# Optimization experiments

Measured on AMD Instinct MI355X. Metric: run time of the kernel, lower is better.

## Reference

```python
import jax, jax.numpy as jnp
import numpy as np

B, L, D = 2, 1024, 1024
H, KV, CH = 16, 4, 8          # attn heads, kv heads, context-manager heads
HD = D // H                   # 64
E, K, FF = 8, 2, 4 * D        # experts, top-k, ffn hidden
DC = 4                        # conv kernel size
EPS = 1e-6


def setup_inputs() -> dict:
    key = jax.random.key(0)
    ks = jax.random.split(key, 32)
    s = 0.02
    n = lambda k, shp: jax.random.normal(k, shp, jnp.float32) * s
    return {
        'x': jax.random.normal(ks[0], (B, L, D), jnp.float32),
        'mask': jnp.ones((B, L), jnp.int32),
        'w_rms1': jnp.ones((D,), jnp.float32),
        'w_rms2': jnp.ones((D,), jnp.float32),
        'w_rms3': jnp.ones((D,), jnp.float32),
        'w_rms4': jnp.ones((D,), jnp.float32),
        'Wq': n(ks[1], (D, D)), 'Wk': n(ks[2], (D, KV * HD)),
        'Wv': n(ks[3], (D, KV * HD)), 'Wo': n(ks[4], (D, D)),
        'Cq': n(ks[5], (D, D)), 'Ck': n(ks[6], (D, D)),
        'Cv': n(ks[7], (D, D)), 'Co': n(ks[8], (D, D)),
        'Wi': n(ks[9], (D, 2 * D)), 'bi': jnp.zeros((2 * D,), jnp.float32),
        'conv_w': n(ks[10], (D, 1, DC)), 'conv_b': jnp.zeros((D,), jnp.float32),
        'Wod': n(ks[11], (D, D)), 'bod': jnp.zeros((D,), jnp.float32),
        'w_gate': n(ks[12], (E, D)),
        'W1': n(ks[13], (E, D, FF)), 'b1': jnp.zeros((E, FF), jnp.float32),
        'W2': n(ks[14], (E, FF, D)), 'b2': jnp.zeros((E, D), jnp.float32),
    }


def _rmsnorm(x, w):
    rms = jnp.sqrt(jnp.mean(x * x, axis=-1, keepdims=True) + EPS)
    return w * (x / rms)


def _mha(x, mask, Wq, Wk, Wv, Wo, nh, nkv):
    b, l, d = x.shape
    hd = d // nh
    q = (x @ Wq).reshape(b, l, nh, hd)
    k = (x @ Wk).reshape(b, l, nkv, hd)
    v = (x @ Wv).reshape(b, l, nkv, hd)
    if nh != nkv:
        rep = nh // nkv
        k = jnp.repeat(k, rep, axis=2)
        v = jnp.repeat(v, rep, axis=2)
    scores = jnp.einsum('bqhd,bkhd->bhqk', q, k) * (hd ** -0.5)
    scores = jnp.where(mask[:, None, None, :] == 0, -jnp.inf, scores)
    attn = jax.nn.softmax(scores, axis=-1)
    out = jnp.einsum('bhqk,bkhd->bqhd', attn, v).reshape(b, l, d)
    return out @ Wo


def _deltanet(x, Wi, bi, conv_w, conv_b, Wod, bod):
    gv = x @ Wi + bi
    gate, value = jnp.split(gv, 2, axis=-1)
    # depthwise causal conv1d (kernel DC, left pad DC-1, truncated to L)
    v_ncl = jnp.transpose(value, (0, 2, 1))  # [B, D, L]
    conv = jax.lax.conv_general_dilated(
        v_ncl, conv_w, window_strides=(1,), padding=[(DC - 1, 0)],
        feature_group_count=D, dimension_numbers=('NCH', 'OIH', 'NCH'))
    conv = conv + conv_b[None, :, None]
    conv = jnp.transpose(conv, (0, 2, 1))  # [B, L, D]
    gated = conv * jax.nn.silu(gate)
    return gated @ Wod + bod


def _moe(x, w_gate, W1, b1, W2, b2):
    b, l, d = x.shape
    flat = x.reshape(-1, d)                                  # [T, D]
    gate = jax.nn.softmax(flat @ w_gate.T, axis=-1)          # [T, E]
    topk_scores, topk_idx = jax.lax.top_k(gate, K)           # [T, K]
    onehot = jax.nn.one_hot(topk_idx, E, dtype=flat.dtype)   # [T, K, E]
    combine = jnp.sum(topk_scores[..., None] * onehot, axis=1)  # [T, E]
    h = jnp.einsum('td,edh->teh', flat, W1) + b1
    h = jax.nn.gelu(h, approximate=False)
    y = jnp.einsum('teh,ehd->ted', h, W2) + b2
    out = jnp.einsum('ted,te->td', y, combine)
    return out.reshape(b, l, d)


def reference(x, mask, w_rms1, w_rms2, w_rms3, w_rms4,
              Wq, Wk, Wv, Wo, Cq, Ck, Cv, Co,
              Wi, bi, conv_w, conv_b, Wod, bod,
              w_gate, W1, b1, W2, b2):
    # eval mode: dropout = identity. multi_token_pred output is discarded by the block.
    res1 = x
    h = _rmsnorm(x, w_rms1)
    h = res1 + _mha(h, mask, Wq, Wk, Wv, Wo, H, KV)
    res2 = h
    # ContextManager stand-in: 8-head softmax self-attention (source unavailable)
    cm = _mha(h, mask, Cq, Ck, Cv, Co, CH, CH)
    h = res2 + cm
    res3 = h
    g = _rmsnorm(h, w_rms2)
    h = res3 + _deltanet(g, Wi, bi, conv_w, conv_b, Wod, bod)
    res4 = h
    g = _rmsnorm(h, w_rms3)
    h = res4 + _moe(g, w_gate, W1, b1, W2, b2)
    h = _rmsnorm(h, w_rms4)
    return h
```

## Files before the change

kernel.cpp:

```cpp
#include <hip/hip_runtime.h>
#include <hip/hip_bf16.h>
#include <math.h>

#define T_TOK 2048
#define B_SZ 2
#define L_SEQ 1024
#define D_MOD 1024
#define N_H 16
#define N_KV 4
#define N_CH 8
#define N_E 8
#define FF_DIM 4096
#define DC_K 4
#define EPS_F 1e-6f

typedef unsigned short u16;
typedef unsigned int u32;
typedef short s16x8 __attribute__((ext_vector_type(8)));
typedef u16 u16x8 __attribute__((ext_vector_type(8)));
typedef float f32x4 __attribute__((ext_vector_type(4)));
struct alignas(8) U16x4 { u16 a, b, c, d; };

__device__ __forceinline__ float gelu_exact(float x) {
    return 0.5f * x * (1.0f + erff(x * 0.70710678118654752f));
}
__device__ __forceinline__ u16 f2bf(float f) {
    u32 x = __float_as_uint(f);
    return (u16)((x + 0x7fffu + ((x >> 16) & 1u)) >> 16);
}
__device__ __forceinline__ float b2f(u16 u) {
    return __uint_as_float(((u32)u) << 16);
}
__device__ __forceinline__ void gload_lds16(const u16* g, u16* l) {
    __builtin_amdgcn_global_load_lds(
        (const __attribute__((address_space(1))) u32*)g,
        (__attribute__((address_space(3))) u32*)l, 16, 0, 0);
}
__device__ __forceinline__ int swz(int row, int ch, int cpr) {
    return (cpr == 4) ? (ch ^ ((row >> 1) & 3)) : (ch ^ (row & 7));
}

struct TDesc {
    const float* src;
    u16* dst;
    int R, C, dstStride, dstRowOff, tileBase, nPerMat;
};
struct TPack { TDesc d[10]; };

__global__ __launch_bounds__(256) void transpose_all(TPack p) {
    __shared__ float ts[64][65];
    int t = blockIdx.x;
    int i = 0;
#pragma unroll
    for (int j = 1; j < 10; ++j)
        if (t >= p.d[j].tileBase) i = j;
    TDesc d = p.d[i];
    int local = t - d.tileBase;
    int e = local / d.nPerMat;
    local -= e * d.nPerMat;
    int ntx = d.C >> 6;
    int bx = local % ntx, by = local / ntx;
    const float* src = d.src + (size_t)e * d.R * d.C + (size_t)(by * 64) * d.C + bx * 64;
    u16* dst = d.dst + (size_t)e * d.C * d.dstStride +
               (size_t)(d.dstRowOff + bx * 64) * d.dstStride + by * 64;
    int tid = threadIdx.x;
#pragma unroll
    for (int k = 0; k < 4; ++k) {
        int fidx = k * 256 + tid;
        int r = fidx >> 4, c4 = (fidx & 15) << 2;
        float4 v = *(const float4*)(src + (size_t)r * d.C + c4);
        ts[r][c4] = v.x; ts[r][c4 + 1] = v.y; ts[r][c4 + 2] = v.z; ts[r][c4 + 3] = v.w;
    }
    __syncthreads();
#pragma unroll
    for (int k = 0; k < 2; ++k) {
        int idx = k * 256 + tid;
        int c = idx >> 3, r8 = (idx & 7) << 3;
        u16x8 o;
#pragma unroll
        for (int j = 0; j < 8; ++j) o[j] = f2bf(ts[r8 + j][c]);
        *(u16x8*)(dst + (size_t)c * d.dstStride + r8) = o;
    }
}

__global__ __launch_bounds__(256) void rmsnorm_kernel(const float* __restrict__ x,
                                                      const float* __restrict__ w,
                                                      float* __restrict__ fo,
                                                      u16* __restrict__ bo) {
    int row = blockIdx.x;
    int tid = threadIdx.x;
    const float* xr = x + (size_t)row * D_MOD;
    float4 v = ((const float4*)xr)[tid];
    float ss = v.x * v.x + v.y * v.y + v.z * v.z + v.w * v.w;
    __shared__ float red[256];
    red[tid] = ss;
    __syncthreads();
    for (int s = 128; s > 0; s >>= 1) {
        if (tid < s) red[tid] += red[tid + s];
        __syncthreads();
    }
    float inv = 1.0f / sqrtf(red[0] * (1.0f / D_MOD) + EPS_F);
    float4 wv = ((const float4*)w)[tid];
    float4 o;
    o.x = v.x * inv * wv.x;
    o.y = v.y * inv * wv.y;
    o.z = v.z * inv * wv.z;
    o.w = v.w * inv * wv.w;
    if (fo) ((float4*)(fo + (size_t)row * D_MOD))[tid] = o;
    if (bo) {
        U16x4 b;
        b.a = f2bf(o.x); b.b = f2bf(o.y); b.c = f2bf(o.z); b.d = f2bf(o.w);
        *(U16x4*)(bo + (size_t)row * D_MOD + tid * 4) = b;
    }
}

template <int MODE, int GELU, int OUTF, int OUTB, int BM, int BK, int TW>
__global__ __launch_bounds__(256) void mfma_gemm(const u16* __restrict__ A,
                                                 const u16* __restrict__ BT,
                                                 const float* __restrict__ bias,
                                                 const float* __restrict__ res,
                                                 float* __restrict__ C,
                                                 u16* __restrict__ Cb,
                                                 const int* __restrict__ list,
                                                 const int* __restrict__ offs,
                                                 const int* __restrict__ counts,
                                                 int M, int N, int K, int nx,
                                                 const float* __restrict__ tW1,
                                                 const float* __restrict__ tW2,
                                                 u16* __restrict__ tW1T,
                                                 u16* __restrict__ tW2T,
                                                 int tLo, int tHi) {
    constexpr int PWR = BM / 2;
    constexpr int MI = PWR / 16;
    constexpr int NI = 4;
    constexpr int CPR = BK / 8;
    constexpr int AISS = (BM * CPR) / 64;
    constexpr int BISS = (128 * CPR) / 64;
    constexpr int APW = (AISS >= 4) ? (AISS / 4) : 1;
    constexpr int BPW = BISS / 4;
    constexpr int SMG = (2 * BM * BK + 2 * 128 * BK) * 2;
    constexpr int SMT = TW ? (64 * 65 * 4) : 0;
    constexpr int SM = SMG > SMT ? SMG : SMT;
    __shared__ alignas(16) char smem[SM];
    u16* ldsA = (u16*)smem;
    u16* ldsB = ldsA + 2 * BM * BK;
    int tid = threadIdx.x;
    int lane = tid & 63, w = tid >> 6;
    int wr = w >> 1, wc = w & 1;
    int bx, by, e;
    if (MODE == 0) {
        bx = blockIdx.x; by = blockIdx.y; e = 0;
    } else {
        int id = blockIdx.x;
        e = id & 7;
        int r = id >> 3;
        bx = r % nx;
        by = r / nx;
    }
    int cnt, off;
    if (MODE == 0) { cnt = M; off = 0; }
    else { cnt = counts[e]; off = offs[e]; }
    int m0 = by * BM;
    if (m0 < cnt) {
        int n0 = bx * 128;
        const u16* Bt = BT + (size_t)e * (size_t)N * K;

        const u16* aSrc[APW];
        const u16* bSrc[BPW];
#pragma unroll
        for (int jp = 0; jp < APW; ++jp) {
            int ii = (AISS >= 4) ? (jp * 4 + w) : w;
            int ci = ii * 64 + lane;
            int rowA = ci / CPR, ch = ci % CPR;
            int rl = m0 + ((rowA < BM) ? rowA : (BM - 1));
            if (rl >= cnt) rl = cnt - 1;
            size_t ga;
            if (MODE == 1) ga = (size_t)list[off + rl] * K;
            else if (MODE == 2) ga = (size_t)(off + rl) * K;
            else ga = (size_t)rl * K;
            aSrc[jp] = A + ga + (swz(rowA, ch, CPR) << 3);
        }
#pragma unroll
        for (int jp = 0; jp < BPW; ++jp) {
            int ii = jp * 4 + w;
            int ci = ii * 64 + lane;
            int rowB = ci / CPR, ch = ci % CPR;
            bSrc[jp] = Bt + (size_t)(n0 + rowB) * K + (swz(rowB, ch, CPR) << 3);
        }

        auto stage = [&](int buf, int k0) {
#pragma unroll
            for (int jp = 0; jp < APW; ++jp) {
                if (AISS >= 4 || w < AISS) {
                    int ii = (AISS >= 4) ? (jp * 4 + w) : w;
                    gload_lds16(aSrc[jp] + k0, ldsA + buf * (BM * BK) + ii * 512);
                }
            }
#pragma unroll
            for (int jp = 0; jp < BPW; ++jp) {
                int ii = jp * 4 + w;
                gload_lds16(bSrc[jp] + k0, ldsB + buf * (128 * BK) + ii * 512);
            }
        };

        f32x4 acc[MI][NI] = {};
        int r16 = lane & 15, cr = lane >> 4;

        stage(0, 0);
        __syncthreads();
        int cur = 0;
        for (int k0 = 0; k0 < K; k0 += BK) {
            if (k0 + BK < K) stage(cur ^ 1, k0 + BK);
#pragma unroll
            for (int hh = 0; hh < BK / 32; ++hh) {
                s16x8 af[MI], bfr[NI];
#pragma unroll
                for (int mi = 0; mi < MI; ++mi) {
                    int row = wr * PWR + mi * 16 + r16;
                    af[mi] = *(const s16x8*)&ldsA[cur * (BM * BK) + row * BK +
                                                  (swz(row, hh * 4 + cr, CPR) << 3)];
                }
#pragma unroll
                for (int ni = 0; ni < NI; ++ni) {
                    int row = wc * 64 + ni * 16 + r16;
                    bfr[ni] = *(const s16x8*)&ldsB[cur * (128 * BK) + row * BK +
                                                   (swz(row, hh * 4 + cr, CPR) << 3)];
                }
#pragma unroll
                for (int mi = 0; mi < MI; ++mi)
#pragma unroll
                    for (int ni = 0; ni < NI; ++ni)
                        acc[mi][ni] = __builtin_amdgcn_mfma_f32_16x16x32_bf16(
                            af[mi], bfr[ni], acc[mi][ni], 0, 0, 0);
            }
            __syncthreads();
            cur ^= 1;
        }

        const float* bias_e = bias ? (bias + (MODE ? (size_t)e * N : 0)) : nullptr;
#pragma unroll
        for (int mi = 0; mi < MI; ++mi) {
#pragma unroll
            for (int ni = 0; ni < NI; ++ni) {
                int rloc = wr * PWR + mi * 16 + (lane >> 4) * 4;
                int col = n0 + wc * 64 + ni * 16 + (lane & 15);
#pragma unroll
                for (int jj = 0; jj < 4; ++jj) {
                    int rl = m0 + rloc + jj;
                    if (rl >= cnt) continue;
                    float val = acc[mi][ni][jj];
                    if (bias_e) val += bias_e[col];
                    if (GELU) val = gelu_exact(val);
                    size_t crow = (MODE == 0) ? (size_t)rl : (size_t)(off + rl);
                    if (res) val += res[crow * N + col];
                    if (OUTF) C[crow * N + col] = val;
                    if (OUTB) Cb[crow * N + col] = f2bf(val);
                }
            }
        }
    }

    if constexpr (TW) {
        int nb = gridDim.x * gridDim.y;
        int bid = blockIdx.y * gridDim.x + blockIdx.x;
        float (*ts)[65] = (float(*)[65])smem;
        __syncthreads();
        for (int t = tLo + bid; t < tHi; t += nb) {
            const float* src;
            u16* dst;
            int Cc, ds;
            if (t < 8192) {
                int ee = t >> 10, loc = t & 1023;
                int tbx = loc & 63, tby = loc >> 6;
                src = tW1 + (size_t)ee * 1024 * FF_DIM + (size_t)(tby << 6) * FF_DIM + (tbx << 6);
                dst = tW1T + (size_t)ee * FF_DIM * 1024 + (size_t)(tbx << 6) * 1024 + (tby << 6);
                Cc = FF_DIM; ds = 1024;
            } else {
                int tt = t - 8192;
                int ee = tt >> 10, loc = tt & 1023;
                int tbx = loc & 15, tby = loc >> 4;
                src = tW2 + (size_t)ee * FF_DIM * 1024 + (size_t)(tby << 6) * 1024 + (tbx << 6);
                dst = tW2T + (size_t)ee * 1024 * FF_DIM + (size_t)(tbx << 6) * FF_DIM + (tby << 6);
                Cc = 1024; ds = FF_DIM;
            }
#pragma unroll
            for (int k = 0; k < 4; ++k) {
                int fidx = k * 256 + tid;
                int r = fidx >> 4, c4 = (fidx & 15) << 2;
                float4 v = *(const float4*)(src + (size_t)r * Cc + c4);
                ts[r][c4] = v.x; ts[r][c4 + 1] = v.y; ts[r][c4 + 2] = v.z; ts[r][c4 + 3] = v.w;
            }
            __syncthreads();
#pragma unroll
            for (int k = 0; k < 2; ++k) {
                int idx = k * 256 + tid;
                int c = idx >> 3, r8 = (idx & 7) << 3;
                u16x8 o;
#pragma unroll
                for (int j = 0; j < 8; ++j) o[j] = f2bf(ts[r8 + j][c]);
                *(u16x8*)(dst + (size_t)c * ds + r8) = o;
            }
            __syncthreads();
        }
    }
}

template <int HD>
__global__ __launch_bounds__(256) void mfma_attn(const u16* __restrict__ Qb,
                                                 const u16* __restrict__ Kb,
                                                 const u16* __restrict__ Vb,
                                                 u16* __restrict__ O,
                                                 int stride, int ostride,
                                                 int nh, int nkv, float scale) {
    constexpr int KT = 64;
    constexpr int CH = HD / 8;
    constexpr int NF = HD / 32;
    constexpr int ND = HD / 16;
    constexpr int VSTR = 72;
    constexpr int NISS = (64 * CH) / (64 * 4);

    __shared__ u16 Kl[64 * HD];
    __shared__ u16 Vt[HD * VSTR];
    __shared__ u16 Pl[4][16 * 72];

    int tid = threadIdx.x, lane = tid & 63, w = tid >> 6;
    int g = lane >> 4, r16 = lane & 15;
    int q0 = blockIdx.x * 64, h = blockIdx.y, b = blockIdx.z;
    int kvh = h / (nh / nkv);

    const u16* Qp = Qb + (size_t)(b * L_SEQ + q0 + w * 16 + r16) * stride + h * HD + g * 8;
    s16x8 qf[NF];
#pragma unroll
    for (int f = 0; f < NF; ++f) qf[f] = *(const s16x8*)(Qp + f * 32);

    const u16* Kbase = Kb + (size_t)(b * L_SEQ) * stride + (size_t)kvh * HD;
    const u16* Vbase = Vb + (size_t)(b * L_SEQ) * stride + (size_t)kvh * HD;

    int srcOffK[NISS];
#pragma unroll
    for (int i = 0; i < NISS; ++i) {
        int ci = (w * NISS + i) * 64 + lane;
        int row = ci / CH;
        int ch = ci % CH;
        srcOffK[i] = row * stride + ((ch ^ (row & 7)) << 3);
    }

    f32x4 ofr[ND] = {};
    float m_r[4], l_r[4];
#pragma unroll
    for (int r = 0; r < 4; ++r) { m_r[r] = -1e30f; l_r[r] = 0.f; }

    for (int kt = 0; kt < L_SEQ / KT; ++kt) {
        const u16* Ksrc = Kbase + (size_t)(kt * KT) * stride;
        const u16* Vsrc = Vbase + (size_t)(kt * KT) * stride;
        __syncthreads();
#pragma unroll
        for (int i = 0; i < NISS; ++i)
            gload_lds16(Ksrc + srcOffK[i], Kl + (size_t)(w * NISS + i) * 512);
#pragma unroll
        for (int half = 0; half < HD / 64; ++half) {
            int dbase = w * 16 + half * 64;
            u16x8 v0 = *(const u16x8*)(Vsrc + (size_t)lane * stride + dbase);
            u16x8 v1 = *(const u16x8*)(Vsrc + (size_t)lane * stride + dbase + 8);
#pragma unroll
            for (int j = 0; j < 8; ++j) {
                Vt[(dbase + j) * VSTR + lane] = v0[j];
                Vt[(dbase + 8 + j) * VSTR + lane] = v1[j];
            }
        }
        __syncthreads();

        f32x4 s[4];
        __builtin_amdgcn_s_setprio(1);
#pragma unroll
        for (int sub = 0; sub < 4; ++sub) {
            f32x4 acc = {};
#pragma unroll
            for (int f = 0; f < NF; ++f) {
                int row = sub * 16 + r16;
                int chunk = (f * 4 + g) ^ (row & 7);
                s16x8 kf = *(const s16x8*)&Kl[(row * CH + chunk) * 8];
                acc = __builtin_amdgcn_mfma_f32_16x16x32_bf16(qf[f], kf, acc, 0, 0, 0);
            }
            s[sub] = acc;
        }
        __builtin_amdgcn_s_setprio(0);

#pragma unroll
        for (int sub = 0; sub < 4; ++sub)
#pragma unroll
            for (int r = 0; r < 4; ++r) s[sub][r] *= scale;
#pragma unroll
        for (int r = 0; r < 4; ++r) {
            float mx = fmaxf(fmaxf(s[0][r], s[1][r]), fmaxf(s[2][r], s[3][r]));
            mx = fmaxf(mx, __shfl_xor(mx, 1));
            mx = fmaxf(mx, __shfl_xor(mx, 2));
            mx = fmaxf(mx, __shfl_xor(mx, 4));
            mx = fmaxf(mx, __shfl_xor(mx, 8));
            float mo = m_r[r];
            float mn = fmaxf(mo, mx);
            float sc = __expf(mo - mn);
            m_r[r] = mn;
            float sum = 0.f;
#pragma unroll
            for (int sub = 0; sub < 4; ++sub) {
                float e = __expf(s[sub][r] - mn);
                s[sub][r] = e;
                sum += e;
            }
            sum += __shfl_xor(sum, 1);
            sum += __shfl_xor(sum, 2);
            sum += __shfl_xor(sum, 4);
            sum += __shfl_xor(sum, 8);
            l_r[r] = l_r[r] * sc + sum;
#pragma unroll
            for (int dsub = 0; dsub < ND; ++dsub) ofr[dsub][r] *= sc;
        }

        u16* Pw = Pl[w];
#pragma unroll
        for (int sub = 0; sub < 4; ++sub)
#pragma unroll
            for (int r = 0; r < 4; ++r) {
                int q = g * 4 + r;
                int k = sub * 16 + r16;
                Pw[q * 72 + (((k >> 3) ^ (q & 7)) << 3) + (k & 7)] = f2bf(s[sub][r]);
            }
        __syncthreads();

        s16x8 pf[2];
#pragma unroll
        for (int ks = 0; ks < 2; ++ks) {
            int chunk = (ks * 4 + g) ^ (r16 & 7);
            pf[ks] = *(const s16x8*)&Pw[r16 * 72 + chunk * 8];
        }
        __builtin_amdgcn_s_setprio(1);
#pragma unroll
        for (int dsub = 0; dsub < ND; ++dsub)
#pragma unroll
            for (int ks = 0; ks < 2; ++ks) {
                s16x8 vf = *(const s16x8*)&Vt[(dsub * 16 + r16) * VSTR + ks * 32 + g * 8];
                ofr[dsub] = __builtin_amdgcn_mfma_f32_16x16x32_bf16(pf[ks], vf, ofr[dsub], 0, 0, 0);
            }
        __builtin_amdgcn_s_setprio(0);
    }

    float inv[4];
#pragma unroll
    for (int r = 0; r < 4; ++r) inv[r] = 1.0f / l_r[r];
#pragma unroll
    for (int dsub = 0; dsub < ND; ++dsub)
#pragma unroll
        for (int r = 0; r < 4; ++r) {
            int q = q0 + w * 16 + g * 4 + r;
            O[(size_t)(b * L_SEQ + q) * ostride + h * HD + dsub * 16 + r16] =
                f2bf(ofr[dsub][r] * inv[r]);
        }
}

__global__ __launch_bounds__(256) void conv_gate_kernel(const u16* __restrict__ gv,
                                                        const float* __restrict__ cw,
                                                        const float* __restrict__ cb,
                                                        u16* __restrict__ gated) {
    int idx = blockIdx.x * 256 + threadIdx.x;
    if (idx >= T_TOK * D_MOD / 8) return;
    int d8 = (idx & 127) << 3;
    int t = idx >> 7;
    int l = t & (L_SEQ - 1);
    float conv[8];
#pragma unroll
    for (int j = 0; j < 8; ++j) conv[j] = cb[d8 + j];
#pragma unroll
    for (int i = 0; i < DC_K; ++i) {
        int lp = l - (DC_K - 1) + i;
        if (lp >= 0) {
            u16x8 v8 = *(const u16x8*)(gv + (size_t)(t - l + lp) * (2 * D_MOD) + D_MOD + d8);
#pragma unroll
            for (int j = 0; j < 8; ++j) conv[j] += b2f(v8[j]) * cw[(d8 + j) * DC_K + i];
        }
    }
    u16x8 g8 = *(const u16x8*)(gv + (size_t)t * (2 * D_MOD) + d8);
    u16x8 o;
#pragma unroll
    for (int j = 0; j < 8; ++j) {
        float gate = b2f(g8[j]);
        float sig = 1.0f / (1.0f + expf(-gate));
        o[j] = f2bf(conv[j] * (gate * sig));
    }
    *(u16x8*)(gated + (size_t)t * D_MOD + d8) = o;
}

__global__ __launch_bounds__(256) void route_kernel(const float* __restrict__ g,
                                                    const float* __restrict__ wg,
                                                    int* __restrict__ tIdx,
                                                    float* __restrict__ tScore,
                                                    int* __restrict__ counts) {
    int t = blockIdx.x, tid = threadIdx.x;
    __shared__ float gs[D_MOD];
    __shared__ float logits[N_E];
    ((float4*)gs)[tid] = ((const float4*)(g + (size_t)t * D_MOD))[tid];
    __syncthreads();
    int e = tid >> 5, lane = tid & 31;
    const float* w = wg + (size_t)e * D_MOD;
    float p = 0.f;
    for (int d = lane; d < D_MOD; d += 32) p += gs[d] * w[d];
    for (int o = 16; o > 0; o >>= 1) p += __shfl_down(p, o, 32);
    if (lane == 0) logits[e] = p;
    __syncthreads();
    if (tid == 0) {
        float mx = logits[0];
        for (int e2 = 1; e2 < N_E; ++e2) mx = fmaxf(mx, logits[e2]);
        float pe[N_E];
        float Z = 0.f;
        for (int e2 = 0; e2 < N_E; ++e2) {
            pe[e2] = expf(logits[e2] - mx);
            Z += pe[e2];
        }
        int i0 = 0;
        float b0 = pe[0];
        for (int e2 = 1; e2 < N_E; ++e2)
            if (pe[e2] > b0) { b0 = pe[e2]; i0 = e2; }
        int i1 = -1;
        float b1 = -1.f;
        for (int e2 = 0; e2 < N_E; ++e2)
            if (e2 != i0 && pe[e2] > b1) { b1 = pe[e2]; i1 = e2; }
        float invZ = 1.0f / Z;
        tIdx[t * 2] = i0;
        tIdx[t * 2 + 1] = i1;
        tScore[t * 2] = b0 * invZ;
        tScore[t * 2 + 1] = b1 * invZ;
        atomicAdd(&counts[i0], 1);
        atomicAdd(&counts[i1], 1);
    }
}

__global__ void prefix_kernel(const int* __restrict__ counts, int* __restrict__ offs,
                              int* __restrict__ cursor) {
    if (threadIdx.x == 0) {
        int acc = 0;
        for (int e = 0; e < N_E; ++e) {
            offs[e] = acc;
            acc += counts[e];
            cursor[e] = 0;
        }
    }
}

__global__ __launch_bounds__(256) void fill_kernel(const int* __restrict__ tIdx,
                                                   const int* __restrict__ offs,
                                                   int* __restrict__ cursor,
                                                   int* __restrict__ list,
                                                   int* __restrict__ pairRow) {
    int t = blockIdx.x * 256 + threadIdx.x;
    if (t >= T_TOK) return;
    for (int kk = 0; kk < 2; ++kk) {
        int e = tIdx[t * 2 + kk];
        int pos = atomicAdd(&cursor[e], 1);
        int slot = offs[e] + pos;
        list[slot] = t;
        pairRow[t * 2 + kk] = slot;
    }
}

__global__ __launch_bounds__(256) void combine_rms_kernel(const u16* __restrict__ ysel,
                                                          const float* __restrict__ tScore,
                                                          const int* __restrict__ pairRow,
                                                          const float* __restrict__ h,
                                                          const float* __restrict__ w,
                                                          float* __restrict__ out) {
    int row = blockIdx.x;
    int tid = threadIdx.x;
    float4 v = ((const float4*)(h + (size_t)row * D_MOD))[tid];
    int r0 = pairRow[row * 2], r1 = pairRow[row * 2 + 1];
    float s0 = tScore[row * 2], s1 = tScore[row * 2 + 1];
    U16x4 y0 = *(const U16x4*)(ysel + (size_t)r0 * D_MOD + tid * 4);
    U16x4 y1 = *(const U16x4*)(ysel + (size_t)r1 * D_MOD + tid * 4);
    v.x += s0 * b2f(y0.a) + s1 * b2f(y1.a);
    v.y += s0 * b2f(y0.b) + s1 * b2f(y1.b);
    v.z += s0 * b2f(y0.c) + s1 * b2f(y1.c);
    v.w += s0 * b2f(y0.d) + s1 * b2f(y1.d);
    __shared__ float red[256];
    red[tid] = v.x * v.x + v.y * v.y + v.z * v.z + v.w * v.w;
    __syncthreads();
    for (int s = 128; s > 0; s >>= 1) {
        if (tid < s) red[tid] += red[tid + s];
        __syncthreads();
    }
    float inv = 1.0f / sqrtf(red[0] * (1.0f / D_MOD) + EPS_F);
    float4 wv = ((const float4*)w)[tid];
    float4 o;
    o.x = v.x * inv * wv.x;
    o.y = v.y * inv * wv.y;
    o.z = v.z * inv * wv.z;
    o.w = v.w * inv * wv.w;
    ((float4*)(out + (size_t)row * D_MOD))[tid] = o;
}

extern "C" void kernel_launch(void* const* d_in, const int* in_sizes, int n_in,
                              void* d_out, int out_size, void* d_ws, size_t ws_size,
                              hipStream_t stream) {
    const float* x = (const float*)d_in[0];
    const float* w_rms1 = (const float*)d_in[2];
    const float* w_rms2 = (const float*)d_in[3];
    const float* w_rms3 = (const float*)d_in[4];
    const float* w_rms4 = (const float*)d_in[5];
    const float* Wq = (const float*)d_in[6];
    const float* Wk = (const float*)d_in[7];
    const float* Wv = (const float*)d_in[8];
    const float* Wo = (const float*)d_in[9];
    const float* Cq = (const float*)d_in[10];
    const float* Ck = (const float*)d_in[11];
    const float* Cv = (const float*)d_in[12];
    const float* Co = (const float*)d_in[13];
    const float* Wi = (const float*)d_in[14];
    const float* bi = (const float*)d_in[15];
    const float* conv_w = (const float*)d_in[16];
    const float* conv_b = (const float*)d_in[17];
    const float* Wod = (const float*)d_in[18];
    const float* bod = (const float*)d_in[19];
    const float* w_gate = (const float*)d_in[20];
    const float* W1 = (const float*)d_in[21];
    const float* b1 = (const float*)d_in[22];
    const float* W2 = (const float*)d_in[23];
    const float* b2 = (const float*)d_in[24];
    float* out = (float*)d_out;

    char* ws = (char*)d_ws;
    size_t off = 0;
    auto alloc_f = [&](size_t n) { float* p = (float*)(ws + off); off += n * 4; return p; };
    auto alloc_b = [&](size_t n) { u16* p = (u16*)(ws + off); off += n * 2; return p; };

    u16* qkvT = alloc_b((size_t)1536 * 1024);
    u16* cqkvT = alloc_b((size_t)3072 * 1024);
    u16* WoT = alloc_b((size_t)1024 * 1024);
    u16* CoT = alloc_b((size_t)1024 * 1024);
    u16* WiT = alloc_b((size_t)2048 * 1024);
    u16* WodT = alloc_b((size_t)1024 * 1024);
    u16* W1T = alloc_b((size_t)N_E * FF_DIM * 1024);
    u16* W2T = alloc_b((size_t)N_E * 1024 * FF_DIM);
    const size_t TD = (size_t)T_TOK * D_MOD;
    float* h = alloc_f(TD);
    float* nrm = alloc_f(TD);
    u16* nrm_bf = alloc_b(TD);
    u16* h_bf = alloc_b(TD);
    u16* ab_bf = alloc_b(TD);
    u16* qkv_bf = alloc_b((size_t)T_TOK * 3072);
    u16* gv_bf = alloc_b((size_t)T_TOK * 2048);
    u16* hsel = alloc_b((size_t)2 * T_TOK * FF_DIM);
    u16* ysel = alloc_b((size_t)2 * T_TOK * D_MOD);
    int* counts = (int*)(ws + off); off += N_E * 4;
    int* offs = (int*)(ws + off); off += N_E * 4;
    int* cursor = (int*)(ws + off); off += N_E * 4;
    int* tIdx = (int*)(ws + off); off += 2 * T_TOK * 4;
    int* list = (int*)(ws + off); off += 2 * T_TOK * 4;
    int* pairRow = (int*)(ws + off); off += 2 * T_TOK * 4;
    float* tScore = alloc_f(2 * T_TOK);

    TPack tp;
    int tb = 0;
    auto mkd = [&](int i, const float* s, u16* d, int R, int C, int ds, int ro) {
        int per = (C >> 6) * (R >> 6);
        tp.d[i] = TDesc{s, d, R, C, ds, ro, tb, per};
        tb += per;
    };
    mkd(0, Wq, qkvT, 1024, 1024, 1024, 0);
    mkd(1, Wk, qkvT, 1024, 256, 1024, 1024);
    mkd(2, Wv, qkvT, 1024, 256, 1024, 1280);
    mkd(3, Cq, cqkvT, 1024, 1024, 1024, 0);
    mkd(4, Ck, cqkvT, 1024, 1024, 1024, 1024);
    mkd(5, Cv, cqkvT, 1024, 1024, 1024, 2048);
    mkd(6, Wo, WoT, 1024, 1024, 1024, 0);
    mkd(7, Co, CoT, 1024, 1024, 1024, 0);
    mkd(8, Wi, WiT, 1024, 2048, 1024, 0);
    mkd(9, Wod, WodT, 1024, 1024, 1024, 0);
    transpose_all<<<tb, 256, 0, stream>>>(tp);

    rmsnorm_kernel<<<T_TOK, 256, 0, stream>>>(x, w_rms1, nullptr, nrm_bf);
    mfma_gemm<0, 0, 0, 1, 32, 64, 1><<<dim3(12, 64, 1), 256, 0, stream>>>(
        nrm_bf, qkvT, nullptr, nullptr, nullptr, qkv_bf, nullptr, nullptr, nullptr,
        T_TOK, 1536, 1024, 0, W1, W2, W1T, W2T, 0, 2600);
    mfma_attn<64><<<dim3(16, N_H, B_SZ), 256, 0, stream>>>(
        qkv_bf, qkv_bf + 1024, qkv_bf + 1280, ab_bf, 1536, 1024, N_H, N_KV, 0.125f);
    mfma_gemm<0, 0, 1, 1, 32, 64, 1><<<dim3(8, 64, 1), 256, 0, stream>>>(
        ab_bf, WoT, nullptr, x, h, h_bf, nullptr, nullptr, nullptr,
        T_TOK, 1024, 1024, 0, W1, W2, W1T, W2T, 2600, 4300);

    mfma_gemm<0, 0, 0, 1, 32, 64, 1><<<dim3(24, 64, 1), 256, 0, stream>>>(
        h_bf, cqkvT, nullptr, nullptr, nullptr, qkv_bf, nullptr, nullptr, nullptr,
        T_TOK, 3072, 1024, 0, W1, W2, W1T, W2T, 4300, 9500);
    mfma_attn<128><<<dim3(16, N_CH, B_SZ), 256, 0, stream>>>(
        qkv_bf, qkv_bf + 1024, qkv_bf + 2048, ab_bf, 3072, 1024, N_CH, N_CH,
        0.088388347648318447f);
    mfma_gemm<0, 0, 1, 0, 32, 64, 1><<<dim3(8, 64, 1), 256, 0, stream>>>(
        ab_bf, CoT, nullptr, h, h, nullptr, nullptr, nullptr, nullptr,
        T_TOK, 1024, 1024, 0, W1, W2, W1T, W2T, 9500, 11200);

    rmsnorm_kernel<<<T_TOK, 256, 0, stream>>>(h, w_rms2, nullptr, nrm_bf);
    mfma_gemm<0, 0, 0, 1, 32, 64, 1><<<dim3(16, 64, 1), 256, 0, stream>>>(
        nrm_bf, WiT, bi, nullptr, nullptr, gv_bf, nullptr, nullptr, nullptr,
        T_TOK, 2048, 1024, 0, W1, W2, W1T, W2T, 11200, 14684);
    conv_gate_kernel<<<(T_TOK * D_MOD / 8 + 255) / 256, 256, 0, stream>>>(gv_bf, conv_w, conv_b, ab_bf);
    mfma_gemm<0, 0, 1, 0, 32, 64, 1><<<dim3(8, 64, 1), 256, 0, stream>>>(
        ab_bf, WodT, bod, h, h, nullptr, nullptr, nullptr, nullptr,
        T_TOK, 1024, 1024, 0, W1, W2, W1T, W2T, 14684, 16384);

    rmsnorm_kernel<<<T_TOK, 256, 0, stream>>>(h, w_rms3, nrm, nrm_bf);
    hipMemsetAsync(counts, 0, N_E * sizeof(int), stream);
    route_kernel<<<T_TOK, 256, 0, stream>>>(nrm, w_gate, tIdx, tScore, counts);
    prefix_kernel<<<1, 64, 0, stream>>>(counts, offs, cursor);
    fill_kernel<<<(T_TOK + 255) / 256, 256, 0, stream>>>(tIdx, offs, cursor, list, pairRow);
    mfma_gemm<1, 1, 0, 1, 128, 32, 0><<<32 * 16 * 8, 256, 0, stream>>>(
        nrm_bf, W1T, b1, nullptr, nullptr, hsel, list, offs, counts,
        T_TOK, FF_DIM, 1024, 32, nullptr, nullptr, nullptr, nullptr, 0, 0);
    mfma_gemm<2, 0, 0, 1, 32, 64, 0><<<8 * 64 * 8, 256, 0, stream>>>(
        hsel, W2T, b2, nullptr, nullptr, ysel, list, offs, counts,
        T_TOK, 1024, FF_DIM, 8, nullptr, nullptr, nullptr, nullptr, 0, 0);
    combine_rms_kernel<<<T_TOK, 256, 0, stream>>>(ysel, tScore, pairRow, h, w_rms4, out);
}
```

Baseline: 620.3 us.

## Split-K the MoE down-projection GEMM and reduce partials in combine kernel

```diff
diff --git a/kernel.cpp b/kernel.cpp
--- a/kernel.cpp
+++ b/kernel.cpp
@@ -147,9 +147,17 @@
     int tid = threadIdx.x;
     int lane = tid & 63, w = tid >> 6;
     int wr = w >> 1, wc = w & 1;
-    int bx, by, e;
+    int bx, by, e, sk = 0;
     if (MODE == 0) {
         bx = blockIdx.x; by = blockIdx.y; e = 0;
+    } else if (MODE == 3) {
+        int id = blockIdx.x;
+        e = id & 7;
+        int r = id >> 3;
+        sk = r & 1;
+        int q = r >> 1;
+        bx = q % nx;
+        by = q / nx;
     } else {
         int id = blockIdx.x;
         e = id & 7;
@@ -164,6 +172,8 @@
     if (m0 < cnt) {
         int n0 = bx * 128;
         const u16* Bt = BT + (size_t)e * (size_t)N * K;
+        int kLo = 0, kHi = K;
+        if (MODE == 3) { kLo = sk * (K >> 1); kHi = kLo + (K >> 1); }
 
         const u16* aSrc[APW];
         const u16* bSrc[BPW];
@@ -176,7 +186,7 @@
             if (rl >= cnt) rl = cnt - 1;
             size_t ga;
             if (MODE == 1) ga = (size_t)list[off + rl] * K;
-            else if (MODE == 2) ga = (size_t)(off + rl) * K;
+            else if (MODE >= 2) ga = (size_t)(off + rl) * K;
             else ga = (size_t)rl * K;
             aSrc[jp] = A + ga + (swz(rowA, ch, CPR) << 3);
         }
@@ -206,11 +216,11 @@
         f32x4 acc[MI][NI] = {};
         int r16 = lane & 15, cr = lane >> 4;
 
-        stage(0, 0);
+        stage(0, kLo);
         __syncthreads();
         int cur = 0;
-        for (int k0 = 0; k0 < K; k0 += BK) {
-            if (k0 + BK < K) stage(cur ^ 1, k0 + BK);
+        for (int k0 = kLo; k0 < kHi; k0 += BK) {
+            if (k0 + BK < kHi) stage(cur ^ 1, k0 + BK);
 #pragma unroll
             for (int hh = 0; hh < BK / 32; ++hh) {
                 s16x8 af[MI], bfr[NI];
@@ -237,7 +247,9 @@
             cur ^= 1;
         }
 
-        const float* bias_e = bias ? (bias + (MODE ? (size_t)e * N : 0)) : nullptr;
+        const float* bias_e = bias ? (bias + ((MODE && MODE != 3) ? (size_t)e * N : 0)) : nullptr;
+        float* Cp = C ? (C + (MODE == 3 ? (size_t)sk * ((size_t)2 * T_TOK * 1024) : (size_t)0))
+                      : nullptr;
 #pragma unroll
         for (int mi = 0; mi < MI; ++mi) {
 #pragma unroll
@@ -253,7 +265,7 @@
                     if (GELU) val = gelu_exact(val);
                     size_t crow = (MODE == 0) ? (size_t)rl : (size_t)(off + rl);
                     if (res) val += res[crow * N + col];
-                    if (OUTF) C[crow * N + col] = val;
+                    if (OUTF) Cp[crow * N + col] = val;
                     if (OUTB) Cb[crow * N + col] = f2bf(val);
                 }
             }
@@ -562,23 +574,31 @@
     }
 }
 
-__global__ __launch_bounds__(256) void combine_rms_kernel(const u16* __restrict__ ysel,
+__global__ __launch_bounds__(256) void combine_rms_kernel(const float* __restrict__ yp,
+                                                          const float* __restrict__ b2,
                                                           const float* __restrict__ tScore,
                                                           const int* __restrict__ pairRow,
+                                                          const int* __restrict__ tIdx,
                                                           const float* __restrict__ h,
                                                           const float* __restrict__ w,
                                                           float* __restrict__ out) {
+    const size_t HALF = (size_t)2 * T_TOK * D_MOD;
     int row = blockIdx.x;
     int tid = threadIdx.x;
     float4 v = ((const float4*)(h + (size_t)row * D_MOD))[tid];
-    int r0 = pairRow[row * 2], r1 = pairRow[row * 2 + 1];
-    float s0 = tScore[row * 2], s1 = tScore[row * 2 + 1];
-    U16x4 y0 = *(const U16x4*)(ysel + (size_t)r0 * D_MOD + tid * 4);
-    U16x4 y1 = *(const U16x4*)(ysel + (size_t)r1 * D_MOD + tid * 4);
-    v.x += s0 * b2f(y0.a) + s1 * b2f(y1.a);
-    v.y += s0 * b2f(y0.b) + s1 * b2f(y1.b);
-    v.z += s0 * b2f(y0.c) + s1 * b2f(y1.c);
-    v.w += s0 * b2f(y0.d) + s1 * b2f(y1.d);
+#pragma unroll
+    for (int kk = 0; kk < 2; ++kk) {
+        int r = pairRow[row * 2 + kk];
+        int e = tIdx[row * 2 + kk];
+        float s = tScore[row * 2 + kk];
+        float4 y0 = ((const float4*)(yp + (size_t)r * D_MOD))[tid];
+        float4 y1 = ((const float4*)(yp + HALF + (size_t)r * D_MOD))[tid];
+        float4 bb = ((const float4*)(b2 + (size_t)e * D_MOD))[tid];
+        v.x += s * (y0.x + y1.x + bb.x);
+        v.y += s * (y0.y + y1.y + bb.y);
+        v.z += s * (y0.z + y1.z + bb.z);
+        v.w += s * (y0.w + y1.w + bb.w);
+    }
     __shared__ float red[256];
     red[tid] = v.x * v.x + v.y * v.y + v.z * v.z + v.w * v.w;
     __syncthreads();
@@ -647,7 +667,7 @@
     u16* qkv_bf = alloc_b((size_t)T_TOK * 3072);
     u16* gv_bf = alloc_b((size_t)T_TOK * 2048);
     u16* hsel = alloc_b((size_t)2 * T_TOK * FF_DIM);
-    u16* ysel = alloc_b((size_t)2 * T_TOK * D_MOD);
+    float* ypart = alloc_f((size_t)2 * 2 * T_TOK * D_MOD);
     int* counts = (int*)(ws + off); off += N_E * 4;
     int* offs = (int*)(ws + off); off += N_E * 4;
     int* cursor = (int*)(ws + off); off += N_E * 4;
@@ -712,8 +732,9 @@
     mfma_gemm<1, 1, 0, 1, 128, 32, 0><<<32 * 16 * 8, 256, 0, stream>>>(
         nrm_bf, W1T, b1, nullptr, nullptr, hsel, list, offs, counts,
         T_TOK, FF_DIM, 1024, 32, nullptr, nullptr, nullptr, nullptr, 0, 0);
-    mfma_gemm<2, 0, 0, 1, 32, 64, 0><<<8 * 64 * 8, 256, 0, stream>>>(
-        hsel, W2T, b2, nullptr, nullptr, ysel, list, offs, counts,
+    mfma_gemm<3, 0, 1, 0, 64, 32, 0><<<2 * 8 * 32 * 8, 256, 0, stream>>>(
+        hsel, W2T, nullptr, nullptr, ypart, nullptr, list, offs, counts,
         T_TOK, 1024, FF_DIM, 8, nullptr, nullptr, nullptr, nullptr, 0, 0);
-    combine_rms_kernel<<<T_TOK, 256, 0, stream>>>(ysel, tScore, pairRow, h, w_rms4, out);
-}
+    combine_rms_kernel<<<T_TOK, 256, 0, stream>>>(ypart, b2, tScore, pairRow, tIdx, h,
+                                                  w_rms4, out);
+}
```

Result: faster. 586.7 us (-5.4%).
